# Kernel tuning notes

Measured on AMD Instinct MI355X. Metric: run time of the kernel, lower is better.

Reference implementation:

```python
import jax, jax.numpy as jnp
import numpy as np

BS, Z, NOBJ = 16384, 512, 64


def setup_inputs() -> dict:
    key = jax.random.key(0)
    ks = jax.random.split(key, 12)
    din = Z + 4  # z concatenated with bounds (x_size = 0)

    def lin(k, i, o):
        kw, kb = jax.random.split(k)
        w = jax.random.normal(kw, (i, o), jnp.float32) * (1.0 / np.sqrt(i))
        b = jax.random.normal(kb, (o,), jnp.float32) * 0.01
        return w, b

    W1, c1 = lin(ks[0], din, 512)
    W2, c2 = lin(ks[1], 512, 256)
    W3, c3 = lin(ks[2], 256, 128)
    W4, c4 = lin(ks[3], 128, 64)
    W5, c5 = lin(ks[4], 64, NOBJ * 4)
    z = jax.random.normal(ks[5], (BS, Z), jnp.float32)
    # room bounds [x_min, y_min, x_max, y_max]; must allow gaps >= 1
    bounds = jnp.array([0.0, 0.0, 40.0, 40.0], jnp.float32)
    return {"z": z, "bounds": bounds,
            "W1": W1, "c1": c1, "W2": W2, "c2": c2, "W3": W3, "c3": c3,
            "W4": W4, "c4": c4, "W5": W5, "c5": c5}


def _lrelu(v):
    return jnp.where(v > 0, v, 0.2 * v)


def _solve_axis(pp, pg, lo, hi):
    """Exact KKT solution of: min (x-pp)^2 + (g-pg)^2  s.t. x>=lo, g>=1, x+g<=hi.
    Returns (x, w) with w = x + g. Matches the parabolic QP per object/axis."""
    x0 = jnp.maximum(pp, lo)          # box projection (lower bounds only)
    g0 = jnp.maximum(pg, 1.0)
    t = 0.5 * (hi - pp - pg)          # projection of (pp,pg) onto line x+g=hi
    xl = jnp.clip(pp + t, lo, hi - 1.0)
    over = (x0 + g0) > hi             # coupling constraint active?
    x = jnp.where(over, xl, x0)
    g = jnp.where(over, hi - xl, g0)
    return x, x + g


def reference(z, bounds, W1, c1, W2, c2, W3, c3, W4, c4, W5, c5):
    bs = z.shape[0]
    bnd = jnp.broadcast_to(bounds, (bs, 4))
    h = jnp.concatenate([z, bnd], axis=1)          # (bs, z_size+4)
    h = _lrelu(h @ W1 + c1)                        # dropout treated as eval/identity
    h = _lrelu(h @ W2 + c2)
    h = _lrelu(h @ W3 + c3)
    h = _lrelu(h @ W4 + c4)
    p = (h @ W5 + c5).reshape(bs, NOBJ, 4)         # per-object params [px, py, pw, ph]
    px, py, pw, ph = p[..., 0], p[..., 1], p[..., 2], p[..., 3]
    b0, b1, b2, b3 = bounds[0], bounds[1], bounds[2], bounds[3]
    # QP objective: sum (x-px)^2+(y-py)^2+((w-x)-pw)^2+((h-y)-ph)^2
    # s.t. x>=b0, y>=b1, w<=b2, h<=b3, x<=w-1, y<=h-1. Separable per object/axis.
    xs, ws = _solve_axis(px, pw, b0, b2)
    ys, hs = _solve_axis(py, ph, b1, b3)
    return jnp.stack([xs, ys, ws, hs], axis=-1)    # (bs, num_objs, 4)
```

## Files before the change

### kernel.cpp

```cpp
#include <hip/hip_runtime.h>


#define MROWS 16384

typedef __attribute__((ext_vector_type(8))) short bf16x8;
typedef __attribute__((ext_vector_type(4))) float floatx4;

__device__ __forceinline__ unsigned short f2bf(float x) {
    union { float f; unsigned u; } c; c.f = x;
    unsigned r = c.u + 0x7fffu + ((c.u >> 16) & 1u);
    return (unsigned short)(r >> 16);
}
__device__ __forceinline__ float bf2f(unsigned short b) {
    union { unsigned u; float f; } c; c.u = ((unsigned)b) << 16;
    return c.f;
}

__global__ __launch_bounds__(256) void pack_wt(
    const float* __restrict__ W1, unsigned short* __restrict__ T1,
    const float* __restrict__ W2, unsigned short* __restrict__ T2,
    const float* __restrict__ W3, unsigned short* __restrict__ T3,
    const float* __restrict__ W4, unsigned short* __restrict__ T4)
{
    const float* W; unsigned short* T; int Kreal, KS, nshift;
    switch (blockIdx.y) {
        case 0:  W = W1; T = T1; Kreal = 516; KS = 17; nshift = 9; break;
        case 1:  W = W2; T = T2; Kreal = 512; KS = 16; nshift = 8; break;
        case 2:  W = W3; T = T3; Kreal = 256; KS = 8;  nshift = 7; break;
        default: W = W4; T = T4; Kreal = 128; KS = 4;  nshift = 6; break;
    }
    const int N = 1 << nshift;
    const int idx = blockIdx.x * 256 + threadIdx.x;
    if (idx >= N * KS * 32) return;
    const int k = idx >> nshift;
    const int n = idx & (N - 1);
    const unsigned short v = (k < Kreal) ? f2bf(W[idx]) : (unsigned short)0;
    const int ntile = n >> 4, m_l = n & 15;
    const int ks = k >> 5, quad = (k >> 3) & 3, e = k & 7;
    T[(size_t)(((ntile * KS + ks) * 64) + quad * 16 + m_l) * 8 + e] = v;
}

#define OFF_ZS   0
#define LD_ZS    552
#define OFF_H1   17664
#define LD_H1    520
#define OFF_H2   0
#define LD_H2    264
#define OFF_H3   17664
#define LD_H3    136
#define OFF_H4   8448
#define LD_H4    72
#define LDS_TOT  34304

template<int NF, int KSTEPS>
__device__ __forceinline__ void layer_gemm(
    unsigned short* lds, int offA, int lda, int offC, int ldc,
    const unsigned short* __restrict__ Wt,
    const float* __restrict__ bias, int wid, int lane)
{
    const int m_l = lane & 15, quad = lane >> 4;
    const unsigned short* __restrict__ Wl =
        Wt + ((size_t)(wid * NF) * KSTEPS * 64 + lane) * 8;
    floatx4 acc[2][NF];
    #pragma unroll
    for (int i = 0; i < 2; ++i)
        #pragma unroll
        for (int j = 0; j < NF; ++j)
            acc[i][j] = (floatx4){0.f, 0.f, 0.f, 0.f};

    #pragma unroll
    for (int ks = 0; ks < KSTEPS; ++ks) {
        const bf16x8 a0 = *(const bf16x8*)&lds[offA + (m_l     ) * lda + ks*32 + quad*8];
        const bf16x8 a1 = *(const bf16x8*)&lds[offA + (m_l + 16) * lda + ks*32 + quad*8];
        #pragma unroll
        for (int j = 0; j < NF; ++j) {
            const bf16x8 b = *(const bf16x8*)(Wl + (size_t)(j * KSTEPS + ks) * 512);
            acc[0][j] = __builtin_amdgcn_mfma_f32_16x16x32_bf16(a0, b, acc[0][j], 0, 0, 0);
            acc[1][j] = __builtin_amdgcn_mfma_f32_16x16x32_bf16(a1, b, acc[1][j], 0, 0, 0);
        }
    }
    #pragma unroll
    for (int j = 0; j < NF; ++j) {
        const int col = wid * (NF * 16) + j * 16 + m_l;
        const float bv = bias[col];
        #pragma unroll
        for (int i = 0; i < 2; ++i)
            #pragma unroll
            for (int r = 0; r < 4; ++r) {
                float v = acc[i][j][r] + bv;
                v = v > 0.f ? v : 0.2f * v;
                lds[offC + (i*16 + quad*4 + r) * ldc + col] = f2bf(v);
            }
    }
}

__global__ __launch_bounds__(512, 4) void fused_mlp_qp(
    const float* __restrict__ z, const float* __restrict__ bounds,
    const unsigned short* __restrict__ Wt1, const float* __restrict__ c1,
    const unsigned short* __restrict__ Wt2, const float* __restrict__ c2,
    const unsigned short* __restrict__ Wt3, const float* __restrict__ c3,
    const unsigned short* __restrict__ Wt4, const float* __restrict__ c4,
    const float* __restrict__ W5, const float* __restrict__ c5,
    float* __restrict__ out)
{
    __shared__ unsigned short lds[LDS_TOT];
    const int tid  = threadIdx.x;
    const int wid  = tid >> 6, lane = tid & 63;
    const int m_l  = lane & 15, quad = lane >> 4;
    const int bm   = blockIdx.x * 32;

    const float4 bnd = *(const float4*)bounds;

    {
        const float4* __restrict__ zf = (const float4*)(z + (size_t)bm * 512);
        #pragma unroll
        for (int i = 0; i < 8; ++i) {
            const int f   = i * 512 + tid;
            const int row = f >> 7, c4 = f & 127;
            const float4 v = zf[f];
            unsigned short t4[4] = {f2bf(v.x), f2bf(v.y), f2bf(v.z), f2bf(v.w)};
            *(uint2*)&lds[OFF_ZS + row * LD_ZS + c4 * 4] = *(uint2*)t4;
        }
        if (tid < 160) {
            const int row = tid / 5, j = tid % 5;
            unsigned short t8[8] = {0,0,0,0,0,0,0,0};
            if (j == 0) { t8[0] = f2bf(bnd.x); t8[1] = f2bf(bnd.y);
                          t8[2] = f2bf(bnd.z); t8[3] = f2bf(bnd.w); }
            *(uint4*)&lds[OFF_ZS + row * LD_ZS + 512 + j * 8] = *(uint4*)t8;
        }
    }
    __syncthreads();

    layer_gemm<4,17>(lds, OFF_ZS, LD_ZS, OFF_H1, LD_H1, Wt1, c1, wid, lane);
    __syncthreads();
    layer_gemm<2,16>(lds, OFF_H1, LD_H1, OFF_H2, LD_H2, Wt2, c2, wid, lane);
    __syncthreads();
    layer_gemm<1,8 >(lds, OFF_H2, LD_H2, OFF_H3, LD_H3, Wt3, c3, wid, lane);
    __syncthreads();
    {
        const int wm4 = wid >> 2, wn4 = wid & 3;
        const unsigned short* __restrict__ Wl4 =
            Wt4 + ((size_t)(wn4 * 4) * 64 + lane) * 8;
        floatx4 acc4 = (floatx4){0.f, 0.f, 0.f, 0.f};
        #pragma unroll
        for (int ks = 0; ks < 4; ++ks) {
            const bf16x8 a = *(const bf16x8*)&lds[OFF_H3 + (wm4*16 + m_l) * LD_H3 + ks*32 + quad*8];
            const bf16x8 b = *(const bf16x8*)(Wl4 + (size_t)ks * 512);
            acc4 = __builtin_amdgcn_mfma_f32_16x16x32_bf16(a, b, acc4, 0, 0, 0);
        }
        const int col = wn4 * 16 + m_l;
        const float bv = c4[col];
        #pragma unroll
        for (int r = 0; r < 4; ++r) {
            float v = acc4[r] + bv;
            v = v > 0.f ? v : 0.2f * v;
            lds[OFF_H4 + (wm4*16 + quad*4 + r) * LD_H4 + col] = f2bf(v);
        }
    }
    __syncthreads();

    const float4 cc = ((const float4*)c5)[lane];
    float ax[4], ay[4], aw[4], ah[4];
    #pragma unroll
    for (int r = 0; r < 4; ++r) { ax[r] = cc.x; ay[r] = cc.y; aw[r] = cc.z; ah[r] = cc.w; }
    const float4* __restrict__ W5v = (const float4*)W5;
    const int rbase = wid * 4;

    #pragma unroll 2
    for (int k4 = 0; k4 < 64; k4 += 4) {
        unsigned short hs[4][4];
        #pragma unroll
        for (int r = 0; r < 4; ++r) {
            const ushort4 t = *(const ushort4*)&lds[OFF_H4 + (rbase + r) * LD_H4 + k4];
            hs[r][0] = t.x; hs[r][1] = t.y; hs[r][2] = t.z; hs[r][3] = t.w;
        }
        #pragma unroll
        for (int kk = 0; kk < 4; ++kk) {
            const float4 w = W5v[(size_t)(k4 + kk) * 64 + lane];
            #pragma unroll
            for (int r = 0; r < 4; ++r) {
                const float h = bf2f(hs[r][kk]);
                ax[r] = fmaf(h, w.x, ax[r]);
                ay[r] = fmaf(h, w.y, ay[r]);
                aw[r] = fmaf(h, w.z, aw[r]);
                ah[r] = fmaf(h, w.w, ah[r]);
            }
        }
    }

    const float b0 = bnd.x, b1 = bnd.y, b2 = bnd.z, b3 = bnd.w;
    #pragma unroll
    for (int r = 0; r < 4; ++r) {
        float xs, wo, ys, ho;
        {
            const float px = ax[r], pw = aw[r];
            const float x0 = fmaxf(px, b0);
            const float g0 = fmaxf(pw, 1.0f);
            const float t  = 0.5f * (b2 - px - pw);
            const float xl = fminf(fmaxf(px + t, b0), b2 - 1.0f);
            const bool over = (x0 + g0) > b2;
            const float x = over ? xl : x0;
            const float g = over ? (b2 - xl) : g0;
            xs = x; wo = x + g;
        }
        {
            const float py = ay[r], ph = ah[r];
            const float x0 = fmaxf(py, b1);
            const float g0 = fmaxf(ph, 1.0f);
            const float t  = 0.5f * (b3 - py - ph);
            const float xl = fminf(fmaxf(py + t, b1), b3 - 1.0f);
            const bool over = (x0 + g0) > b3;
            const float x = over ? xl : x0;
            const float g = over ? (b3 - xl) : g0;
            ys = x; ho = x + g;
        }
        float4 o; o.x = xs; o.y = ys; o.z = wo; o.w = ho;
        ((float4*)out)[(size_t)(bm + rbase + r) * 64 + lane] = o;
    }
}

extern "C" void kernel_launch(void* const* d_in, const int* in_sizes, int n_in,
                              void* d_out, int out_size, void* d_ws, size_t ws_size,
                              hipStream_t stream) {
    const float* z      = (const float*)d_in[0];
    const float* bounds = (const float*)d_in[1];
    const float* W1 = (const float*)d_in[2];
    const float* c1 = (const float*)d_in[3];
    const float* W2 = (const float*)d_in[4];
    const float* c2 = (const float*)d_in[5];
    const float* W3 = (const float*)d_in[6];
    const float* c3 = (const float*)d_in[7];
    const float* W4 = (const float*)d_in[8];
    const float* c4 = (const float*)d_in[9];
    const float* W5 = (const float*)d_in[10];
    const float* c5 = (const float*)d_in[11];
    float* out = (float*)d_out;

    unsigned short* ws  = (unsigned short*)d_ws;
    unsigned short* Wt1 = ws;
    unsigned short* Wt2 = Wt1 + 278528;
    unsigned short* Wt3 = Wt2 + 131072;
    unsigned short* Wt4 = Wt3 + 32768;

    pack_wt<<<dim3(1088, 4), 256, 0, stream>>>(W1, Wt1, W2, Wt2, W3, Wt3, W4, Wt4);
    fused_mlp_qp<<<dim3(MROWS / 32), 512, 0, stream>>>(
        z, bounds, Wt1, c1, Wt2, c2, Wt3, c3, Wt4, c4, W5, c5, out);
}
```

Measured before the change: 141.1 us.

## Stage weight tiles into LDS via global_load_lds double buffering

Replaces direct per-wave global loads of packed bf16 weight fragments with async global-to-LDS DMA into a double-buffered weight region. Each K-step's tile for the next step is prefetched while the current one feeds the MFMAs, with a block barrier per step. LDS use roughly doubles and launch bounds drop from 4 to 2 blocks per CU, which lowers occupancy and adds many __syncthreads. Activation buffer offsets are rearranged to make room for the weight buffer.

```diff
diff --git a/kernel.cpp b/kernel.cpp
--- a/kernel.cpp
+++ b/kernel.cpp
@@ -14,6 +14,12 @@
 __device__ __forceinline__ float bf2f(unsigned short b) {
     union { unsigned u; float f; } c; c.u = ((unsigned)b) << 16;
     return c.f;
+}
+
+__device__ __forceinline__ void dma16(const unsigned short* g, unsigned short* l, int lane) {
+    __builtin_amdgcn_global_load_lds(
+        (const __attribute__((address_space(1))) void*)(g + (size_t)lane * 8),
+        (__attribute__((address_space(3))) void*)(l), 16, 0, 0);
 }
 
 __global__ __launch_bounds__(256) void pack_wt(
@@ -46,55 +52,15 @@
 #define LD_H1    520
 #define OFF_H2   0
 #define LD_H2    264
-#define OFF_H3   17664
+#define OFF_H3   8448
 #define LD_H3    136
-#define OFF_H4   8448
+#define OFF_H4   12800
 #define LD_H4    72
-#define LDS_TOT  34304
-
-template<int NF, int KSTEPS>
-__device__ __forceinline__ void layer_gemm(
-    unsigned short* lds, int offA, int lda, int offC, int ldc,
-    const unsigned short* __restrict__ Wt,
-    const float* __restrict__ bias, int wid, int lane)
-{
-    const int m_l = lane & 15, quad = lane >> 4;
-    const unsigned short* __restrict__ Wl =
-        Wt + ((size_t)(wid * NF) * KSTEPS * 64 + lane) * 8;
-    floatx4 acc[2][NF];
-    #pragma unroll
-    for (int i = 0; i < 2; ++i)
-        #pragma unroll
-        for (int j = 0; j < NF; ++j)
-            acc[i][j] = (floatx4){0.f, 0.f, 0.f, 0.f};
-
-    #pragma unroll
-    for (int ks = 0; ks < KSTEPS; ++ks) {
-        const bf16x8 a0 = *(const bf16x8*)&lds[offA + (m_l     ) * lda + ks*32 + quad*8];
-        const bf16x8 a1 = *(const bf16x8*)&lds[offA + (m_l + 16) * lda + ks*32 + quad*8];
-        #pragma unroll
-        for (int j = 0; j < NF; ++j) {
-            const bf16x8 b = *(const bf16x8*)(Wl + (size_t)(j * KSTEPS + ks) * 512);
-            acc[0][j] = __builtin_amdgcn_mfma_f32_16x16x32_bf16(a0, b, acc[0][j], 0, 0, 0);
-            acc[1][j] = __builtin_amdgcn_mfma_f32_16x16x32_bf16(a1, b, acc[1][j], 0, 0, 0);
-        }
-    }
-    #pragma unroll
-    for (int j = 0; j < NF; ++j) {
-        const int col = wid * (NF * 16) + j * 16 + m_l;
-        const float bv = bias[col];
-        #pragma unroll
-        for (int i = 0; i < 2; ++i)
-            #pragma unroll
-            for (int r = 0; r < 4; ++r) {
-                float v = acc[i][j][r] + bv;
-                v = v > 0.f ? v : 0.2f * v;
-                lds[offC + (i*16 + quad*4 + r) * ldc + col] = f2bf(v);
-            }
-    }
-}
-
-__global__ __launch_bounds__(512, 4) void fused_mlp_qp(
+#define OFF_WB   34304
+#define WB_HALF  16384
+#define LDS_TOT  67072
+
+__global__ __launch_bounds__(512, 2) void fused_mlp_qp(
     const float* __restrict__ z, const float* __restrict__ bounds,
     const unsigned short* __restrict__ Wt1, const float* __restrict__ c1,
     const unsigned short* __restrict__ Wt2, const float* __restrict__ c2,
@@ -112,14 +78,22 @@
     const float4 bnd = *(const float4*)bounds;
 
     {
+        unsigned short* dst = lds + OFF_WB;
+        #pragma unroll
+        for (int i = 0; i < 4; ++i) {
+            const int nt = wid * 4 + i;
+            dma16(Wt1 + (size_t)(nt * 17 + 0) * 64 * 8, dst + nt * 512, lane);
+        }
+    }
+    {
         const float4* __restrict__ zf = (const float4*)(z + (size_t)bm * 512);
         #pragma unroll
         for (int i = 0; i < 8; ++i) {
             const int f   = i * 512 + tid;
-            const int row = f >> 7, c4 = f & 127;
+            const int row = f >> 7, c4i = f & 127;
             const float4 v = zf[f];
             unsigned short t4[4] = {f2bf(v.x), f2bf(v.y), f2bf(v.z), f2bf(v.w)};
-            *(uint2*)&lds[OFF_ZS + row * LD_ZS + c4 * 4] = *(uint2*)t4;
+            *(uint2*)&lds[OFF_ZS + row * LD_ZS + c4i * 4] = *(uint2*)t4;
         }
         if (tid < 160) {
             const int row = tid / 5, j = tid % 5;
@@ -131,21 +105,155 @@
     }
     __syncthreads();
 
-    layer_gemm<4,17>(lds, OFF_ZS, LD_ZS, OFF_H1, LD_H1, Wt1, c1, wid, lane);
-    __syncthreads();
-    layer_gemm<2,16>(lds, OFF_H1, LD_H1, OFF_H2, LD_H2, Wt2, c2, wid, lane);
-    __syncthreads();
-    layer_gemm<1,8 >(lds, OFF_H2, LD_H2, OFF_H3, LD_H3, Wt3, c3, wid, lane);
-    __syncthreads();
-    {
+    {
+        floatx4 acc[2][4];
+        #pragma unroll
+        for (int i = 0; i < 2; ++i)
+            #pragma unroll
+            for (int j = 0; j < 4; ++j) acc[i][j] = (floatx4){0.f,0.f,0.f,0.f};
+
+        #pragma unroll
+        for (int ks = 0; ks < 17; ++ks) {
+            if (ks > 0) __syncthreads();
+            if (ks < 16) {
+                unsigned short* dst = lds + OFF_WB + ((ks + 1) & 1) * WB_HALF;
+                #pragma unroll
+                for (int i = 0; i < 4; ++i) {
+                    const int nt = wid * 4 + i;
+                    dma16(Wt1 + (size_t)(nt * 17 + ks + 1) * 64 * 8, dst + nt * 512, lane);
+                }
+            }
+            const unsigned short* wb = lds + OFF_WB + (ks & 1) * WB_HALF;
+            const bf16x8 a0 = *(const bf16x8*)&lds[OFF_ZS + (m_l     ) * LD_ZS + ks*32 + quad*8];
+            const bf16x8 a1 = *(const bf16x8*)&lds[OFF_ZS + (m_l + 16) * LD_ZS + ks*32 + quad*8];
+            #pragma unroll
+            for (int j = 0; j < 4; ++j) {
+                const bf16x8 b = *(const bf16x8*)(wb + (wid * 4 + j) * 512 + lane * 8);
+                acc[0][j] = __builtin_amdgcn_mfma_f32_16x16x32_bf16(a0, b, acc[0][j], 0, 0, 0);
+                acc[1][j] = __builtin_amdgcn_mfma_f32_16x16x32_bf16(a1, b, acc[1][j], 0, 0, 0);
+            }
+        }
+        #pragma unroll
+        for (int j = 0; j < 4; ++j) {
+            const int col = wid * 64 + j * 16 + m_l;
+            const float bv = c1[col];
+            #pragma unroll
+            for (int i = 0; i < 2; ++i)
+                #pragma unroll
+                for (int r = 0; r < 4; ++r) {
+                    float v = acc[i][j][r] + bv;
+                    v = v > 0.f ? v : 0.2f * v;
+                    lds[OFF_H1 + (i*16 + quad*4 + r) * LD_H1 + col] = f2bf(v);
+                }
+        }
+    }
+    __syncthreads();
+
+    {
+        {
+            unsigned short* dst = lds + OFF_WB;
+            #pragma unroll
+            for (int i = 0; i < 4; ++i) {
+                const int nt = wid * 2 + (i >> 1), kl = i & 1;
+                dma16(Wt2 + (size_t)(nt * 16 + kl) * 64 * 8, dst + (nt * 2 + kl) * 512, lane);
+            }
+        }
+        __syncthreads();
+
+        floatx4 acc[2][2];
+        #pragma unroll
+        for (int i = 0; i < 2; ++i)
+            #pragma unroll
+            for (int j = 0; j < 2; ++j) acc[i][j] = (floatx4){0.f,0.f,0.f,0.f};
+
+        #pragma unroll
+        for (int c = 0; c < 8; ++c) {
+            if (c > 0) __syncthreads();
+            if (c < 7) {
+                unsigned short* dst = lds + OFF_WB + ((c + 1) & 1) * WB_HALF;
+                #pragma unroll
+                for (int i = 0; i < 4; ++i) {
+                    const int nt = wid * 2 + (i >> 1), kl = i & 1;
+                    dma16(Wt2 + (size_t)(nt * 16 + (c + 1) * 2 + kl) * 64 * 8,
+                          dst + (nt * 2 + kl) * 512, lane);
+                }
+            }
+            const unsigned short* wb = lds + OFF_WB + (c & 1) * WB_HALF;
+            #pragma unroll
+            for (int kl = 0; kl < 2; ++kl) {
+                const int ks = c * 2 + kl;
+                const bf16x8 a0 = *(const bf16x8*)&lds[OFF_H1 + (m_l     ) * LD_H1 + ks*32 + quad*8];
+                const bf16x8 a1 = *(const bf16x8*)&lds[OFF_H1 + (m_l + 16) * LD_H1 + ks*32 + quad*8];
+                #pragma unroll
+                for (int j = 0; j < 2; ++j) {
+                    const bf16x8 b = *(const bf16x8*)(wb + ((wid*2 + j)*2 + kl)*512 + lane*8);
+                    acc[0][j] = __builtin_amdgcn_mfma_f32_16x16x32_bf16(a0, b, acc[0][j], 0, 0, 0);
+                    acc[1][j] = __builtin_amdgcn_mfma_f32_16x16x32_bf16(a1, b, acc[1][j], 0, 0, 0);
+                }
+            }
+        }
+        #pragma unroll
+        for (int j = 0; j < 2; ++j) {
+            const int col = wid * 32 + j * 16 + m_l;
+            const float bv = c2[col];
+            #pragma unroll
+            for (int i = 0; i < 2; ++i)
+                #pragma unroll
+                for (int r = 0; r < 4; ++r) {
+                    float v = acc[i][j][r] + bv;
+                    v = v > 0.f ? v : 0.2f * v;
+                    lds[OFF_H2 + (i*16 + quad*4 + r) * LD_H2 + col] = f2bf(v);
+                }
+        }
+    }
+    __syncthreads();
+
+    {
+        #pragma unroll
+        for (int i = 0; i < 8; ++i) {
+            dma16(Wt3 + (size_t)(wid * 8 + i) * 64 * 8,
+                  lds + OFF_WB + (wid * 8 + i) * 512, lane);
+        }
+        __syncthreads();
+
+        floatx4 acc[2];
+        acc[0] = (floatx4){0.f,0.f,0.f,0.f};
+        acc[1] = (floatx4){0.f,0.f,0.f,0.f};
+        #pragma unroll
+        for (int ks = 0; ks < 8; ++ks) {
+            const bf16x8 a0 = *(const bf16x8*)&lds[OFF_H2 + (m_l     ) * LD_H2 + ks*32 + quad*8];
+            const bf16x8 a1 = *(const bf16x8*)&lds[OFF_H2 + (m_l + 16) * LD_H2 + ks*32 + quad*8];
+            const bf16x8 b  = *(const bf16x8*)(lds + OFF_WB + (wid * 8 + ks) * 512 + lane * 8);
+            acc[0] = __builtin_amdgcn_mfma_f32_16x16x32_bf16(a0, b, acc[0], 0, 0, 0);
+            acc[1] = __builtin_amdgcn_mfma_f32_16x16x32_bf16(a1, b, acc[1], 0, 0, 0);
+        }
+        const int col = wid * 16 + m_l;
+        const float bv = c3[col];
+        #pragma unroll
+        for (int i = 0; i < 2; ++i)
+            #pragma unroll
+            for (int r = 0; r < 4; ++r) {
+                float v = acc[i][r] + bv;
+                v = v > 0.f ? v : 0.2f * v;
+                lds[OFF_H3 + (i*16 + quad*4 + r) * LD_H3 + col] = f2bf(v);
+            }
+    }
+    __syncthreads();
+
+    {
+        #pragma unroll
+        for (int i = 0; i < 2; ++i) {
+            const int f = wid * 2 + i;
+            dma16(Wt4 + (size_t)f * 64 * 8, lds + OFF_WB + f * 512, lane);
+        }
+        __syncthreads();
+
         const int wm4 = wid >> 2, wn4 = wid & 3;
-        const unsigned short* __restrict__ Wl4 =
-            Wt4 + ((size_t)(wn4 * 4) * 64 + lane) * 8;
-        floatx4 acc4 = (floatx4){0.f, 0.f, 0.f, 0.f};
+        floatx4 acc4 = (floatx4){0.f,0.f,0.f,0.f};
         #pragma unroll
         for (int ks = 0; ks < 4; ++ks) {
             const bf16x8 a = *(const bf16x8*)&lds[OFF_H3 + (wm4*16 + m_l) * LD_H3 + ks*32 + quad*8];
-            const bf16x8 b = *(const bf16x8*)(Wl4 + (size_t)ks * 512);
+            const bf16x8 b = *(const bf16x8*)(lds + OFF_WB + (wn4 * 4 + ks) * 512 + lane * 8);
             acc4 = __builtin_amdgcn_mfma_f32_16x16x32_bf16(a, b, acc4, 0, 0, 0);
         }
         const int col = wn4 * 16 + m_l;
```

Result: slower. 147.8 us (+4.8%).
